# Kernel optimization log

Measured on AMD Instinct MI355X. Metric: run time of the kernel, lower is better.

Reference implementation:

```python
import jax, jax.numpy as jnp
import numpy as np

ROUTE_NUM = 3
EPS = 1e-8


def squash(s):
    # s: [bs, J, d2]; squash along last dim
    sq = jnp.sum(s * s, axis=-1, keepdims=True)
    return (sq / (1.0 + sq)) * s / jnp.sqrt(sq + EPS)


def setup_inputs() -> dict:
    key = jax.random.key(0)
    k1, k2, k3 = jax.random.split(key, 3)
    bs, in_dim, s1 = 64, 256, 16
    out_dim, J = 32, 64           # J = num_out_caps (as_final_output)
    I = s1 * s1                   # num_in_caps = 256
    x = jax.random.normal(k1, (bs, in_dim, s1, s1), dtype=jnp.float32)
    b_init = jax.random.uniform(k2, (bs, J, I), dtype=jnp.float32)
    W = jax.random.normal(k3, (out_dim * J, in_dim), dtype=jnp.float32) * 0.05
    Wb = jnp.zeros((out_dim * J,), dtype=jnp.float32)
    return {"x": x, "b_init": b_init, "W": W, "Wb": Wb}


def reference(x, b_init, W, Wb):
    bs = x.shape[0]
    J, I = b_init.shape[1], b_init.shape[2]
    d2 = W.shape[0] // J
    # 1x1 conv == per-pixel GEMM: [bs, OUT, s1, s1]
    pred = jnp.einsum('oi,bihw->bohw', W, x) + Wb[None, :, None, None]
    # [bs, J, d2, I] -> [bs, I, J, d2]
    pred = pred.reshape(bs, J, d2, I).transpose(0, 3, 1, 2)
    b = b_init
    v = None
    for _ in range(ROUTE_NUM):
        c = jax.nn.softmax(b, axis=1)                  # softmax over out-caps J
        s = jnp.einsum('bji,bijd->bjd', c, pred)       # weighted sum over in-caps
        v = squash(s)                                  # [bs, J, d2]
        db = jax.lax.stop_gradient(jnp.einsum('bjd,bijd->bji', v, pred))
        b = b + db
    return v
```

## Files before the change

### kernel.cpp

```cpp
#include <hip/hip_runtime.h>
#include <hip/hip_bf16.h>

#define BS    64
#define KDIM  256
#define ICAP  256
#define JCAP  64
#define D2    32
#define OUTD  2048
#define NPART 16

typedef short bf16x8 __attribute__((ext_vector_type(8)));
typedef float f32x4  __attribute__((ext_vector_type(4)));

static __device__ __forceinline__ float bf2f(unsigned u16) {
  union { unsigned u; float f; } v; v.u = u16 << 16; return v.f;
}
static __device__ __forceinline__ unsigned short f2bf(float x) {
  union { float f; unsigned u; } v; v.f = x;
  unsigned r = v.u + 0x7fffu + ((v.u >> 16) & 1u);
  return (unsigned short)(r >> 16);
}
static __device__ __forceinline__ void unpack8(uint4 u, float* f) {
  f[0] = bf2f(u.x & 0xffffu); f[1] = bf2f(u.x >> 16);
  f[2] = bf2f(u.y & 0xffffu); f[3] = bf2f(u.y >> 16);
  f[4] = bf2f(u.z & 0xffffu); f[5] = bf2f(u.z >> 16);
  f[6] = bf2f(u.w & 0xffffu); f[7] = bf2f(u.w >> 16);
}
static __device__ __forceinline__ void gl_lds16(const unsigned short* g,
                                                unsigned short* l) {
  __builtin_amdgcn_global_load_lds(
      (const __attribute__((address_space(1))) unsigned int*)g,
      (__attribute__((address_space(3))) unsigned int*)l, 16, 0, 0);
}

__global__ __launch_bounds__(256) void prep(
    const float* __restrict__ W, const float* __restrict__ x,
    const float* __restrict__ Binit,
    unsigned short* __restrict__ Wbf, unsigned short* __restrict__ xT,
    unsigned short* __restrict__ c0)
{
  __shared__ union {
    float Ls[64][65];
    float Bs[64][68];
  } sm;
  const int t   = threadIdx.x;
  const int blk = blockIdx.x;

  if (blk < 256) {
    const int g = blk * 256 + t;
    const float* s = W + (size_t)g * 8;
    f32x4 a = *(const f32x4*)s;
    f32x4 b = *(const f32x4*)(s + 4);
    uint4 o;
    o.x = (unsigned)f2bf(a.x) | ((unsigned)f2bf(a.y) << 16);
    o.y = (unsigned)f2bf(a.z) | ((unsigned)f2bf(a.w) << 16);
    o.z = (unsigned)f2bf(b.x) | ((unsigned)f2bf(b.y) << 16);
    o.w = (unsigned)f2bf(b.z) | ((unsigned)f2bf(b.w) << 16);
    *(uint4*)(Wbf + (size_t)g * 8) = o;
  } else if (blk < 1280) {
    const int bid = blk - 256;
    const int i0  = (bid & 3) * 64;
    const int k0  = ((bid >> 2) & 3) * 64;
    const int b   = bid >> 4;
    for (int it = 0; it < 4; ++it) {
      const int k  = it * 16 + (t >> 4);
      const int i4 = (t & 15) * 4;
      f32x4 v = *(const f32x4*)(x + ((size_t)(b * KDIM + k0 + k) * ICAP) + i0 + i4);
      sm.Ls[k][i4 + 0] = v.x; sm.Ls[k][i4 + 1] = v.y;
      sm.Ls[k][i4 + 2] = v.z; sm.Ls[k][i4 + 3] = v.w;
    }
    __syncthreads();
    const int i  = t >> 2;
    const int kc = (t & 3) * 16;
    unsigned pk[8];
    for (int q = 0; q < 8; ++q) {
      float lo = sm.Ls[kc + 2 * q][i];
      float hi = sm.Ls[kc + 2 * q + 1][i];
      pk[q] = (unsigned)f2bf(lo) | ((unsigned)f2bf(hi) << 16);
    }
    unsigned short* dst = xT + ((size_t)(b * ICAP + i0 + i) * KDIM) + k0 + kc;
    uint4 s0; s0.x = pk[0]; s0.y = pk[1]; s0.z = pk[2]; s0.w = pk[3];
    uint4 s1; s1.x = pk[4]; s1.y = pk[5]; s1.z = pk[6]; s1.w = pk[7];
    *(uint4*)dst       = s0;
    *(uint4*)(dst + 8) = s1;
  } else {
    const int bid = blk - 1280;
    const int b   = bid >> 2;
    const int q   = bid & 3;
    {
      const int j  = t >> 2;
      const int c4 = (t & 3) * 16;
      const float* src = Binit + ((size_t)(b * JCAP + j) * ICAP) + q * 64 + c4;
      for (int r = 0; r < 4; ++r) {
        f32x4 v = *(const f32x4*)(src + r * 4);
        *(f32x4*)&sm.Bs[j][c4 + r * 4] = v;
      }
    }
    __syncthreads();
    if (t < 64) {
      const int ii = t;
      float m = -3.0e38f;
      for (int j = 0; j < 64; ++j) m = fmaxf(m, sm.Bs[j][ii]);
      float se = 0.f;
      for (int j = 0; j < 64; ++j) se += __expf(sm.Bs[j][ii] - m);
      const float inv = 1.0f / se;
      unsigned short* dst = c0 + ((size_t)(b * ICAP + q * 64 + ii) * JCAP);
      for (int qq = 0; qq < 8; ++qq) {
        unsigned pk[4];
        for (int h = 0; h < 4; ++h) {
          float lo = __expf(sm.Bs[qq * 8 + 2 * h][ii] - m) * inv;
          float hi = __expf(sm.Bs[qq * 8 + 2 * h + 1][ii] - m) * inv;
          pk[h] = (unsigned)f2bf(lo) | ((unsigned)f2bf(hi) << 16);
        }
        uint4 s; s.x = pk[0]; s.y = pk[1]; s.z = pk[2]; s.w = pk[3];
        *(uint4*)(dst + qq * 8) = s;
      }
    }
  }
}

__global__ __launch_bounds__(256) void gemm_pred(
    const unsigned short* __restrict__ Wbf,
    const unsigned short* __restrict__ xT,
    const float* __restrict__ Wb,
    const unsigned short* __restrict__ c0,
    unsigned short* __restrict__ P,
    float* __restrict__ s0part)
{
  __shared__ union {
    unsigned short AB[2][128][64];
    struct {
      unsigned short C[128][136];
      unsigned short c0t[128][4];
    } ep;
  } sm;

  const int tid = threadIdx.x;
  const int b   = blockIdx.z;
  const int o0  = blockIdx.x * 128;
  const int i0  = blockIdx.y * 128;
  const int l   = tid & 63;
  const int m   = l & 15;
  const int w   = tid >> 6;
  const int wo  = (w & 1) * 64;
  const int wi  = (w >> 1) * 64;

  const int srow = l >> 3;
  const int gch  = (l & 7) ^ srow;

  f32x4 acc[4][4];
  for (int a = 0; a < 4; ++a)
    for (int c = 0; c < 4; ++c) acc[a][c] = (f32x4){0.f, 0.f, 0.f, 0.f};

  for (int r = 0; r < 4; ++r) {
    const int k0 = r * 64;
    __syncthreads();
    for (int c = 0; c < 4; ++c) {
      const int q   = w * 4 + c;
      const int row = q * 8 + srow;
      gl_lds16(Wbf + (size_t)(o0 + row) * KDIM + k0 + gch * 8,
               &sm.AB[0][q * 8][0]);
      gl_lds16(xT + ((size_t)(b * ICAP + i0 + row) * KDIM) + k0 + gch * 8,
               &sm.AB[1][q * 8][0]);
    }
    __syncthreads();
    for (int ks = 0; ks < 2; ++ks) {
      const int clog = ks * 4 + (l >> 4);
      bf16x8 af[4], bfg[4];
      for (int ti = 0; ti < 4; ++ti) {
        const int row = wo + 16 * ti + m;
        af[ti] = *(const bf16x8*)&sm.AB[0][row][(clog ^ (m & 7)) * 8];
      }
      for (int tj = 0; tj < 4; ++tj) {
        const int row = wi + 16 * tj + m;
        bfg[tj] = *(const bf16x8*)&sm.AB[1][row][(clog ^ (m & 7)) * 8];
      }
      for (int ti = 0; ti < 4; ++ti)
        for (int tj = 0; tj < 4; ++tj)
          acc[ti][tj] = __builtin_amdgcn_mfma_f32_16x16x32_bf16(
              af[ti], bfg[tj], acc[ti][tj], 0, 0, 0);
    }
  }

  __syncthreads();
  {
    const int q4 = (l >> 4) * 4;
    for (int ti = 0; ti < 4; ++ti) {
      const int ob = wo + 16 * ti + q4;
      f32x4 wb4 = *(const f32x4*)(Wb + o0 + ob);
      for (int tj = 0; tj < 4; ++tj) {
        const int ii = wi + 16 * tj + m;
        f32x4 a = acc[ti][tj];
        uint2 pk;
        pk.x = (unsigned)f2bf(a.x + wb4.x) | ((unsigned)f2bf(a.y + wb4.y) << 16);
        pk.y = (unsigned)f2bf(a.z + wb4.z) | ((unsigned)f2bf(a.w + wb4.w) << 16);
        *(uint2*)&sm.ep.C[ii][ob] = pk;
      }
    }
  }
  if (tid < 128) {
    const int j0 = blockIdx.x * 4;
    uint2 v = *(const uint2*)(c0 + ((size_t)(b * ICAP + i0 + tid) * JCAP) + j0);
    *(uint2*)&sm.ep.c0t[tid][0] = v;
  }
  __syncthreads();
  for (int rr = 0; rr < 8; ++rr) {
    const int id  = rr * 256 + tid;
    const int row = id >> 4;
    const int seg = id & 15;
    uint4 v = *(const uint4*)&sm.ep.C[row][seg * 8];
    *(uint4*)(P + ((size_t)(b * ICAP + i0 + row) * OUTD) + o0 + seg * 8) = v;
  }
  {
    const int oc = tid & 127;
    const int h  = tid >> 7;
    const int jj = oc >> 5;
    float s = 0.f;
    for (int ii = 0; ii < 64; ++ii) {
      const int i = h * 64 + ii;
      s += bf2f(sm.ep.C[i][oc]) * bf2f(sm.ep.c0t[i][jj]);
    }
    const int p = blockIdx.y * 2 + h;
    s0part[((size_t)(b * 4 + p) * OUTD) + o0 + oc] = s;
  }
}

__global__ __launch_bounds__(256) void route_fused(
    const unsigned short* __restrict__ P,
    const float* __restrict__ Binit,
    float* __restrict__ B1,
    const float* __restrict__ part_in,
    const int npart_in,
    float* __restrict__ part_out,
    const int pass)
{
  __shared__ union {
    float Vs[2112];
    float Ps[4][2112];
  } sm;

  const int tid = threadIdx.x;
  const int l   = tid & 63;
  const int w   = tid >> 6;
  const int b   = blockIdx.x >> 4;
  const int g   = blockIdx.x & 15;

  {
    const float* base = part_in + (size_t)b * npart_in * OUTD + tid * 8;
    float s[8] = {0.f,0.f,0.f,0.f,0.f,0.f,0.f,0.f};
    for (int p = 0; p < npart_in; ++p) {
      f32x4 a = *(const f32x4*)(base + (size_t)p * OUTD);
      f32x4 c = *(const f32x4*)(base + (size_t)p * OUTD + 4);
      s[0] += a.x; s[1] += a.y; s[2] += a.z; s[3] += a.w;
      s[4] += c.x; s[5] += c.y; s[6] += c.z; s[7] += c.w;
    }
    float sq = 0.f;
    for (int c = 0; c < 8; ++c) sq += s[c] * s[c];
    sq += __shfl_xor(sq, 1, 64);
    sq += __shfl_xor(sq, 2, 64);
    float scale = (sq / (1.0f + sq)) / sqrtf(sq + 1e-8f);
    const int j  = tid >> 2;
    const int d0 = (tid & 3) * 8;
    for (int c = 0; c < 8; ++c) sm.Vs[j * 33 + d0 + c] = scale * s[c];
  }
  __syncthreads();
  float vv[32];
  for (int k = 0; k < 32; ++k) vv[k] = sm.Vs[l * 33 + k];

  const int i0 = g * 16 + w * 4;
  float bold[4];
  if (pass == 1) {
    f32x4 t = *(const f32x4*)(Binit + (size_t)(b * JCAP + l) * ICAP + i0);
    bold[0] = t.x; bold[1] = t.y; bold[2] = t.z; bold[3] = t.w;
  } else {
    for (int ii = 0; ii < 4; ++ii)
      bold[ii] = B1[((size_t)(b * ICAP + i0 + ii)) * JCAP + l];
  }

  float sacc[32];
  for (int k = 0; k < 32; ++k) sacc[k] = 0.f;

  const unsigned short* pbase = P + ((size_t)(b * ICAP + i0) * OUTD) + l * D2;
  uint4 ubuf[2][4];
  for (int q = 0; q < 4; ++q) ubuf[0][q] = *(const uint4*)(pbase + q * 8);
  for (int q = 0; q < 4; ++q) ubuf[1][q] = *(const uint4*)(pbase + OUTD + q * 8);

#pragma unroll
  for (int ii = 0; ii < 4; ++ii) {
    uint4 cur[4];
    for (int q = 0; q < 4; ++q) cur[q] = ubuf[ii & 1][q];
    if (ii + 2 < 4)
      for (int q = 0; q < 4; ++q)
        ubuf[ii & 1][q] = *(const uint4*)(pbase + (size_t)(ii + 2) * OUTD + q * 8);

    float db = 0.f;
    for (int q = 0; q < 4; ++q) {
      float ps[8]; unpack8(cur[q], ps);
      for (int k = 0; k < 8; ++k) db += ps[k] * vv[q * 8 + k];
    }
    float bnew = bold[ii] + db;
    if (pass == 1) B1[((size_t)(b * ICAP + i0 + ii)) * JCAP + l] = bnew;

    float mx = bnew;
    for (int off = 1; off < 64; off <<= 1) mx = fmaxf(mx, __shfl_xor(mx, off, 64));
    float e = __expf(bnew - mx);
    float se = e;
    for (int off = 1; off < 64; off <<= 1) se += __shfl_xor(se, off, 64);
    float c = e / se;
    for (int q = 0; q < 4; ++q) {
      float ps[8]; unpack8(cur[q], ps);
      for (int k = 0; k < 8; ++k) sacc[q * 8 + k] += c * ps[k];
    }
  }

  __syncthreads();
  for (int k = 0; k < 32; ++k) sm.Ps[w][l * 33 + k] = sacc[k];
  __syncthreads();

  {
    const int o0 = tid * 8;
    float s[8];
    for (int c = 0; c < 8; ++c) {
      const int o = o0 + c, j = o >> 5, d = o & 31, idx = j * 33 + d;
      s[c] = sm.Ps[0][idx] + sm.Ps[1][idx] + sm.Ps[2][idx] + sm.Ps[3][idx];
    }
    float* dst = part_out + ((size_t)(b * NPART + g)) * OUTD + o0;
    f32x4 t0 = {s[0], s[1], s[2], s[3]};
    f32x4 t1 = {s[4], s[5], s[6], s[7]};
    *(f32x4*)dst       = t0;
    *(f32x4*)(dst + 4) = t1;
  }
}

__global__ __launch_bounds__(256) void squash_final(
    const float* __restrict__ part,
    float* __restrict__ outp)
{
  const int tid = threadIdx.x;
  const int b   = blockIdx.x;
  const float* base = part + (size_t)b * NPART * OUTD + tid * 8;
  float s[8] = {0.f,0.f,0.f,0.f,0.f,0.f,0.f,0.f};
  for (int p = 0; p < NPART; ++p) {
    f32x4 a = *(const f32x4*)(base + (size_t)p * OUTD);
    f32x4 c = *(const f32x4*)(base + (size_t)p * OUTD + 4);
    s[0] += a.x; s[1] += a.y; s[2] += a.z; s[3] += a.w;
    s[4] += c.x; s[5] += c.y; s[6] += c.z; s[7] += c.w;
  }
  float sq = 0.f;
  for (int c = 0; c < 8; ++c) sq += s[c] * s[c];
  sq += __shfl_xor(sq, 1, 64);
  sq += __shfl_xor(sq, 2, 64);
  float scale = (sq / (1.0f + sq)) / sqrtf(sq + 1e-8f);
  float* dst = outp + (size_t)b * OUTD + tid * 8;
  f32x4 t0 = {scale*s[0], scale*s[1], scale*s[2], scale*s[3]};
  f32x4 t1 = {scale*s[4], scale*s[5], scale*s[6], scale*s[7]};
  *(f32x4*)dst       = t0;
  *(f32x4*)(dst + 4) = t1;
}

extern "C" void kernel_launch(void* const* d_in, const int* in_sizes, int n_in,
                              void* d_out, int out_size, void* d_ws, size_t ws_size,
                              hipStream_t stream) {
  const float* x  = (const float*)d_in[0];
  const float* bi = (const float*)d_in[1];
  const float* W  = (const float*)d_in[2];
  const float* Wb = (const float*)d_in[3];
  float* out = (float*)d_out;

  char* ws = (char*)d_ws;
  const size_t MiB = 1024 * 1024;
  unsigned short* P        = (unsigned short*)ws;
  unsigned short* xT       = (unsigned short*)(ws + 64 * MiB);
  float*          partial1 = (float*)(ws + 64 * MiB);
  unsigned short* Wbf      = (unsigned short*)(ws + 72 * MiB);
  unsigned short* c0       = (unsigned short*)(ws + 73 * MiB);
  float*          s0part   = (float*)(ws + 75 * MiB);
  float*          partial2 = (float*)(ws + 72 * MiB);
  float* B1                = (float*)(ws + 80 * MiB);

  prep<<<dim3(1536), 256, 0, stream>>>(W, x, bi, Wbf, xT, c0);
  gemm_pred<<<dim3(16, 2, 64), 256, 0, stream>>>(Wbf, xT, Wb, c0, P, s0part);
  route_fused<<<dim3(1024), 256, 0, stream>>>(P, bi, B1, s0part, 4, partial1, 1);
  route_fused<<<dim3(1024), 256, 0, stream>>>(P, bi, B1, partial1, NPART, partial2, 2);
  squash_final<<<dim3(64), 256, 0, stream>>>(partial2, out);
}
```

Baseline: 157.5 us.

## Avoid materializing prediction tensor by reassociating routing through x and W

The old version built the full bf16 prediction tensor P [bs, I, OUT] with a GEMM and streamed it twice during routing. The new version reassociates the algebra. s = W·(x·cᵀ) + Wb·Σc is computed via a small MFMA product of x with the coupling matrix followed by a W contraction. The logit update db = (vᵀW)·x is computed by forming U = vᵀW, split into hi/lo bf16 parts, and then running an MFMA against xT. This removes the 64 MiB intermediate and its memory traffic, at the cost of more kernel launches (nine instead of five), only 256-block grids, and some scalar W-contraction loops.

New measurement: 206.8 us. 1.31x slower.

```diff
diff --git a/kernel.cpp b/kernel.cpp
--- a/kernel.cpp
+++ b/kernel.cpp
@@ -1,5 +1,4 @@
 #include <hip/hip_runtime.h>
-#include <hip/hip_bf16.h>
 
 #define BS    64
 #define KDIM  256
@@ -7,7 +6,6 @@
 #define JCAP  64
 #define D2    32
 #define OUTD  2048
-#define NPART 16
 
 typedef short bf16x8 __attribute__((ext_vector_type(8)));
 typedef float f32x4  __attribute__((ext_vector_type(4)));
@@ -26,22 +24,17 @@
   f[4] = bf2f(u.z & 0xffffu); f[5] = bf2f(u.z >> 16);
   f[6] = bf2f(u.w & 0xffffu); f[7] = bf2f(u.w >> 16);
 }
-static __device__ __forceinline__ void gl_lds16(const unsigned short* g,
-                                                unsigned short* l) {
-  __builtin_amdgcn_global_load_lds(
-      (const __attribute__((address_space(1))) unsigned int*)g,
-      (__attribute__((address_space(3))) unsigned int*)l, 16, 0, 0);
-}
 
 __global__ __launch_bounds__(256) void prep(
     const float* __restrict__ W, const float* __restrict__ x,
     const float* __restrict__ Binit,
     unsigned short* __restrict__ Wbf, unsigned short* __restrict__ xT,
-    unsigned short* __restrict__ c0)
+    unsigned short* __restrict__ xKI, unsigned short* __restrict__ c0,
+    float* __restrict__ cpart)
 {
   __shared__ union {
     float Ls[64][65];
-    float Bs[64][68];
+    struct { float Bs[64][68]; float mx[64]; float inv[64]; } S;
   } sm;
   const int t   = threadIdx.x;
   const int blk = blockIdx.x;
@@ -70,19 +63,36 @@
       sm.Ls[k][i4 + 2] = v.z; sm.Ls[k][i4 + 3] = v.w;
     }
     __syncthreads();
-    const int i  = t >> 2;
-    const int kc = (t & 3) * 16;
-    unsigned pk[8];
-    for (int q = 0; q < 8; ++q) {
-      float lo = sm.Ls[kc + 2 * q][i];
-      float hi = sm.Ls[kc + 2 * q + 1][i];
-      pk[q] = (unsigned)f2bf(lo) | ((unsigned)f2bf(hi) << 16);
-    }
-    unsigned short* dst = xT + ((size_t)(b * ICAP + i0 + i) * KDIM) + k0 + kc;
-    uint4 s0; s0.x = pk[0]; s0.y = pk[1]; s0.z = pk[2]; s0.w = pk[3];
-    uint4 s1; s1.x = pk[4]; s1.y = pk[5]; s1.z = pk[6]; s1.w = pk[7];
-    *(uint4*)dst       = s0;
-    *(uint4*)(dst + 8) = s1;
+    {
+      const int i  = t >> 2;
+      const int kc = (t & 3) * 16;
+      unsigned pk[8];
+      for (int q = 0; q < 8; ++q) {
+        float lo = sm.Ls[kc + 2 * q][i];
+        float hi = sm.Ls[kc + 2 * q + 1][i];
+        pk[q] = (unsigned)f2bf(lo) | ((unsigned)f2bf(hi) << 16);
+      }
+      unsigned short* dst = xT + ((size_t)(b * ICAP + i0 + i) * KDIM) + k0 + kc;
+      uint4 s0; s0.x = pk[0]; s0.y = pk[1]; s0.z = pk[2]; s0.w = pk[3];
+      uint4 s1; s1.x = pk[4]; s1.y = pk[5]; s1.z = pk[6]; s1.w = pk[7];
+      *(uint4*)dst       = s0;
+      *(uint4*)(dst + 8) = s1;
+    }
+    {
+      const int k   = t >> 2;
+      const int ic4 = (t & 3) * 16;
+      unsigned pk[8];
+      for (int h = 0; h < 8; ++h) {
+        float lo = sm.Ls[k][ic4 + 2 * h];
+        float hi = sm.Ls[k][ic4 + 2 * h + 1];
+        pk[h] = (unsigned)f2bf(lo) | ((unsigned)f2bf(hi) << 16);
+      }
+      unsigned short* dst = xKI + ((size_t)(b * KDIM + k0 + k) * ICAP) + i0 + ic4;
+      uint4 s0; s0.x = pk[0]; s0.y = pk[1]; s0.z = pk[2]; s0.w = pk[3];
+      uint4 s1; s1.x = pk[4]; s1.y = pk[5]; s1.z = pk[6]; s1.w = pk[7];
+      *(uint4*)dst       = s0;
+      *(uint4*)(dst + 8) = s1;
+    }
   } else {
     const int bid = blk - 1280;
     const int b   = bid >> 2;
@@ -91,269 +101,331 @@
       const int j  = t >> 2;
       const int c4 = (t & 3) * 16;
       const float* src = Binit + ((size_t)(b * JCAP + j) * ICAP) + q * 64 + c4;
-      for (int r = 0; r < 4; ++r) {
-        f32x4 v = *(const f32x4*)(src + r * 4);
-        *(f32x4*)&sm.Bs[j][c4 + r * 4] = v;
-      }
+      for (int r = 0; r < 4; ++r)
+        *(f32x4*)&sm.S.Bs[j][c4 + r * 4] = *(const f32x4*)(src + r * 4);
     }
     __syncthreads();
     if (t < 64) {
       const int ii = t;
       float m = -3.0e38f;
-      for (int j = 0; j < 64; ++j) m = fmaxf(m, sm.Bs[j][ii]);
+      for (int j = 0; j < 64; ++j) m = fmaxf(m, sm.S.Bs[j][ii]);
       float se = 0.f;
-      for (int j = 0; j < 64; ++j) se += __expf(sm.Bs[j][ii] - m);
-      const float inv = 1.0f / se;
-      unsigned short* dst = c0 + ((size_t)(b * ICAP + q * 64 + ii) * JCAP);
-      for (int qq = 0; qq < 8; ++qq) {
-        unsigned pk[4];
-        for (int h = 0; h < 4; ++h) {
-          float lo = __expf(sm.Bs[qq * 8 + 2 * h][ii] - m) * inv;
-          float hi = __expf(sm.Bs[qq * 8 + 2 * h + 1][ii] - m) * inv;
-          pk[h] = (unsigned)f2bf(lo) | ((unsigned)f2bf(hi) << 16);
-        }
-        uint4 s; s.x = pk[0]; s.y = pk[1]; s.z = pk[2]; s.w = pk[3];
-        *(uint4*)(dst + qq * 8) = s;
+      for (int j = 0; j < 64; ++j) se += __expf(sm.S.Bs[j][ii] - m);
+      sm.S.mx[ii]  = m;
+      sm.S.inv[ii] = 1.0f / se;
+    }
+    __syncthreads();
+    {
+      const int j  = t >> 2;
+      const int c4 = (t & 3) * 16;
+      float cs = 0.f;
+      unsigned pk[8];
+      for (int h = 0; h < 8; ++h) {
+        const int i0 = c4 + 2 * h;
+        float lo = __expf(sm.S.Bs[j][i0]     - sm.S.mx[i0])     * sm.S.inv[i0];
+        float hi = __expf(sm.S.Bs[j][i0 + 1] - sm.S.mx[i0 + 1]) * sm.S.inv[i0 + 1];
+        cs += lo + hi;
+        pk[h] = (unsigned)f2bf(lo) | ((unsigned)f2bf(hi) << 16);
       }
-    }
-  }
-}
-
-__global__ __launch_bounds__(256) void gemm_pred(
+      unsigned short* dst = c0 + ((size_t)(b * JCAP + j) * ICAP) + q * 64 + c4;
+      uint4 s0; s0.x = pk[0]; s0.y = pk[1]; s0.z = pk[2]; s0.w = pk[3];
+      uint4 s1; s1.x = pk[4]; s1.y = pk[5]; s1.z = pk[6]; s1.w = pk[7];
+      *(uint4*)dst       = s0;
+      *(uint4*)(dst + 8) = s1;
+      cs += __shfl_xor(cs, 1, 64);
+      cs += __shfl_xor(cs, 2, 64);
+      if ((t & 3) == 0) cpart[((size_t)(b * 4 + q)) * JCAP + j] = cs;
+    }
+  }
+}
+
+__global__ __launch_bounds__(256) void k_sv(
+    const unsigned short* __restrict__ xKI,
+    const unsigned short* __restrict__ cmat,
     const unsigned short* __restrict__ Wbf,
-    const unsigned short* __restrict__ xT,
-    const float* __restrict__ Wb,
-    const unsigned short* __restrict__ c0,
-    unsigned short* __restrict__ P,
-    float* __restrict__ s0part)
+    float* __restrict__ spart)
 {
-  __shared__ union {
-    unsigned short AB[2][128][64];
-    struct {
-      unsigned short C[128][136];
-      unsigned short c0t[128][4];
-    } ep;
-  } sm;
-
+  __shared__ float Y[64][68];
   const int tid = threadIdx.x;
-  const int b   = blockIdx.z;
-  const int o0  = blockIdx.x * 128;
-  const int i0  = blockIdx.y * 128;
-  const int l   = tid & 63;
-  const int m   = l & 15;
-  const int w   = tid >> 6;
-  const int wo  = (w & 1) * 64;
-  const int wi  = (w >> 1) * 64;
-
-  const int srow = l >> 3;
-  const int gch  = (l & 7) ^ srow;
-
-  f32x4 acc[4][4];
-  for (int a = 0; a < 4; ++a)
-    for (int c = 0; c < 4; ++c) acc[a][c] = (f32x4){0.f, 0.f, 0.f, 0.f};
-
-  for (int r = 0; r < 4; ++r) {
-    const int k0 = r * 64;
-    __syncthreads();
-    for (int c = 0; c < 4; ++c) {
-      const int q   = w * 4 + c;
-      const int row = q * 8 + srow;
-      gl_lds16(Wbf + (size_t)(o0 + row) * KDIM + k0 + gch * 8,
-               &sm.AB[0][q * 8][0]);
-      gl_lds16(xT + ((size_t)(b * ICAP + i0 + row) * KDIM) + k0 + gch * 8,
-               &sm.AB[1][q * 8][0]);
-    }
-    __syncthreads();
-    for (int ks = 0; ks < 2; ++ks) {
-      const int clog = ks * 4 + (l >> 4);
-      bf16x8 af[4], bfg[4];
-      for (int ti = 0; ti < 4; ++ti) {
-        const int row = wo + 16 * ti + m;
-        af[ti] = *(const bf16x8*)&sm.AB[0][row][(clog ^ (m & 7)) * 8];
-      }
-      for (int tj = 0; tj < 4; ++tj) {
-        const int row = wi + 16 * tj + m;
-        bfg[tj] = *(const bf16x8*)&sm.AB[1][row][(clog ^ (m & 7)) * 8];
-      }
-      for (int ti = 0; ti < 4; ++ti)
-        for (int tj = 0; tj < 4; ++tj)
-          acc[ti][tj] = __builtin_amdgcn_mfma_f32_16x16x32_bf16(
-              af[ti], bfg[tj], acc[ti][tj], 0, 0, 0);
-    }
-  }
-
-  __syncthreads();
-  {
-    const int q4 = (l >> 4) * 4;
-    for (int ti = 0; ti < 4; ++ti) {
-      const int ob = wo + 16 * ti + q4;
-      f32x4 wb4 = *(const f32x4*)(Wb + o0 + ob);
-      for (int tj = 0; tj < 4; ++tj) {
-        const int ii = wi + 16 * tj + m;
-        f32x4 a = acc[ti][tj];
-        uint2 pk;
-        pk.x = (unsigned)f2bf(a.x + wb4.x) | ((unsigned)f2bf(a.y + wb4.y) << 16);
-        pk.y = (unsigned)f2bf(a.z + wb4.z) | ((unsigned)f2bf(a.w + wb4.w) << 16);
-        *(uint2*)&sm.ep.C[ii][ob] = pk;
-      }
-    }
-  }
-  if (tid < 128) {
-    const int j0 = blockIdx.x * 4;
-    uint2 v = *(const uint2*)(c0 + ((size_t)(b * ICAP + i0 + tid) * JCAP) + j0);
-    *(uint2*)&sm.ep.c0t[tid][0] = v;
-  }
-  __syncthreads();
-  for (int rr = 0; rr < 8; ++rr) {
-    const int id  = rr * 256 + tid;
-    const int row = id >> 4;
-    const int seg = id & 15;
-    uint4 v = *(const uint4*)&sm.ep.C[row][seg * 8];
-    *(uint4*)(P + ((size_t)(b * ICAP + i0 + row) * OUTD) + o0 + seg * 8) = v;
-  }
-  {
-    const int oc = tid & 127;
-    const int h  = tid >> 7;
-    const int jj = oc >> 5;
-    float s = 0.f;
-    for (int ii = 0; ii < 64; ++ii) {
-      const int i = h * 64 + ii;
-      s += bf2f(sm.ep.C[i][oc]) * bf2f(sm.ep.c0t[i][jj]);
-    }
-    const int p = blockIdx.y * 2 + h;
-    s0part[((size_t)(b * 4 + p) * OUTD) + o0 + oc] = s;
-  }
-}
-
-__global__ __launch_bounds__(256) void route_fused(
-    const unsigned short* __restrict__ P,
-    const float* __restrict__ Binit,
-    float* __restrict__ B1,
-    const float* __restrict__ part_in,
-    const int npart_in,
-    float* __restrict__ part_out,
-    const int pass)
-{
-  __shared__ union {
-    float Vs[2112];
-    float Ps[4][2112];
-  } sm;
-
-  const int tid = threadIdx.x;
+  const int b   = blockIdx.x >> 2;
+  const int kc  = blockIdx.x & 3;
   const int l   = tid & 63;
   const int w   = tid >> 6;
-  const int b   = blockIdx.x >> 4;
-  const int g   = blockIdx.x & 15;
-
+
+  f32x4 acc[4];
+  for (int n = 0; n < 4; ++n) acc[n] = (f32x4){0.f, 0.f, 0.f, 0.f};
+
+  const unsigned short* Ap =
+      xKI + ((size_t)(b * KDIM + kc * 64 + w * 16 + (l & 15))) * ICAP + (l >> 4) * 8;
+  const unsigned short* Bp =
+      cmat + ((size_t)(b * JCAP + (l & 15))) * ICAP + (l >> 4) * 8;
+#pragma unroll
+  for (int ks = 0; ks < 8; ++ks) {
+    bf16x8 a = *(const bf16x8*)(Ap + ks * 32);
+#pragma unroll
+    for (int n = 0; n < 4; ++n) {
+      bf16x8 bb = *(const bf16x8*)(Bp + (size_t)n * 16 * ICAP + ks * 32);
+      acc[n] = __builtin_amdgcn_mfma_f32_16x16x32_bf16(a, bb, acc[n], 0, 0, 0);
+    }
+  }
+#pragma unroll
+  for (int n = 0; n < 4; ++n)
+#pragma unroll
+    for (int r = 0; r < 4; ++r)
+      Y[w * 16 + (l >> 4) * 4 + r][n * 16 + (l & 15)] = acc[n][r];
+  __syncthreads();
+
+  const int j = tid >> 2;
+  float sacc[8];
+#pragma unroll
+  for (int d = 0; d < 8; ++d) sacc[d] = 0.f;
+  const unsigned short* wbase = Wbf + (size_t)(tid * 8) * KDIM + kc * 64;
+  for (int k8 = 0; k8 < 8; ++k8) {
+    float y8[8];
+#pragma unroll
+    for (int e = 0; e < 8; ++e) y8[e] = Y[k8 * 8 + e][j];
+#pragma unroll
+    for (int d = 0; d < 8; ++d) {
+      uint4 u = *(const uint4*)(wbase + (size_t)d * KDIM + k8 * 8);
+      float f[8]; unpack8(u, f);
+      float s = sacc[d];
+#pragma unroll
+      for (int e = 0; e < 8; ++e) s += f[e] * y8[e];
+      sacc[d] = s;
+    }
+  }
+  float* dst = spart + ((size_t)(b * 4 + kc)) * OUTD + tid * 8;
+  f32x4 t0 = {sacc[0], sacc[1], sacc[2], sacc[3]};
+  f32x4 t1 = {sacc[4], sacc[5], sacc[6], sacc[7]};
+  *(f32x4*)dst       = t0;
+  *(f32x4*)(dst + 4) = t1;
+}
+
+__global__ __launch_bounds__(256) void k_u(
+    const float* __restrict__ spart, const float* __restrict__ cpart,
+    const float* __restrict__ Wb, const unsigned short* __restrict__ Wbf,
+    unsigned short* __restrict__ Uhi, unsigned short* __restrict__ Ulo)
+{
+  __shared__ float vls[JCAP * 33];
+  const int tid = threadIdx.x;
+  const int b   = blockIdx.x >> 2;
+  const int kc  = blockIdx.x & 3;
+  const int j   = tid >> 2;
   {
-    const float* base = part_in + (size_t)b * npart_in * OUTD + tid * 8;
-    float s[8] = {0.f,0.f,0.f,0.f,0.f,0.f,0.f,0.f};
-    for (int p = 0; p < npart_in; ++p) {
-      f32x4 a = *(const f32x4*)(base + (size_t)p * OUTD);
-      f32x4 c = *(const f32x4*)(base + (size_t)p * OUTD + 4);
-      s[0] += a.x; s[1] += a.y; s[2] += a.z; s[3] += a.w;
-      s[4] += c.x; s[5] += c.y; s[6] += c.z; s[7] += c.w;
-    }
+    const float* sp = spart + (size_t)b * 4 * OUTD + tid * 8;
+    f32x4 a0 = *(const f32x4*)sp;
+    f32x4 a1 = *(const f32x4*)(sp + 4);
+    for (int p = 1; p < 4; ++p) {
+      a0 += *(const f32x4*)(sp + (size_t)p * OUTD);
+      a1 += *(const f32x4*)(sp + (size_t)p * OUTD + 4);
+    }
+    float cs = cpart[((size_t)b * 4) * JCAP + j] + cpart[((size_t)(b * 4 + 1)) * JCAP + j] +
+               cpart[((size_t)(b * 4 + 2)) * JCAP + j] + cpart[((size_t)(b * 4 + 3)) * JCAP + j];
+    f32x4 wb0 = *(const f32x4*)(Wb + tid * 8);
+    f32x4 wb1 = *(const f32x4*)(Wb + tid * 8 + 4);
+    float s8[8];
+    s8[0] = a0.x + cs * wb0.x; s8[1] = a0.y + cs * wb0.y;
+    s8[2] = a0.z + cs * wb0.z; s8[3] = a0.w + cs * wb0.w;
+    s8[4] = a1.x + cs * wb1.x; s8[5] = a1.y + cs * wb1.y;
+    s8[6] = a1.z + cs * wb1.z; s8[7] = a1.w + cs * wb1.w;
     float sq = 0.f;
-    for (int c = 0; c < 8; ++c) sq += s[c] * s[c];
+    for (int e = 0; e < 8; ++e) sq += s8[e] * s8[e];
     sq += __shfl_xor(sq, 1, 64);
     sq += __shfl_xor(sq, 2, 64);
     float scale = (sq / (1.0f + sq)) / sqrtf(sq + 1e-8f);
-    const int j  = tid >> 2;
     const int d0 = (tid & 3) * 8;
-    for (int c = 0; c < 8; ++c) sm.Vs[j * 33 + d0 + c] = scale * s[c];
+    for (int e = 0; e < 8; ++e) vls[j * 33 + d0 + e] = scale * s8[e];
   }
   __syncthreads();
-  float vv[32];
-  for (int k = 0; k < 32; ++k) vv[k] = sm.Vs[l * 33 + k];
-
-  const int i0 = g * 16 + w * 4;
-  float bold[4];
+
+  const int kg = kc * 64 + (tid & 3) * 16;
+  float acc[16];
+#pragma unroll
+  for (int e = 0; e < 16; ++e) acc[e] = 0.f;
+  const float* vj = vls + j * 33;
+  const unsigned short* wrow = Wbf + (size_t)(j * D2) * KDIM + kg;
+  for (int d = 0; d < 32; ++d) {
+    float vd = vj[d];
+    uint4 u0 = *(const uint4*)(wrow + (size_t)d * KDIM);
+    uint4 u1 = *(const uint4*)(wrow + (size_t)d * KDIM + 8);
+    float f[16]; unpack8(u0, f); unpack8(u1, f + 8);
+#pragma unroll
+    for (int e = 0; e < 16; ++e) acc[e] += vd * f[e];
+  }
+  unsigned ph[8], pl[8];
+  for (int h = 0; h < 8; ++h) {
+    unsigned short h0 = f2bf(acc[2 * h]), h1 = f2bf(acc[2 * h + 1]);
+    float r0 = acc[2 * h] - bf2f(h0), r1 = acc[2 * h + 1] - bf2f(h1);
+    ph[h] = (unsigned)h0 | ((unsigned)h1 << 16);
+    pl[h] = (unsigned)f2bf(r0) | ((unsigned)f2bf(r1) << 16);
+  }
+  size_t off = ((size_t)(b * JCAP + j)) * KDIM + kg;
+  uint4 q0; q0.x = ph[0]; q0.y = ph[1]; q0.z = ph[2]; q0.w = ph[3];
+  uint4 q1; q1.x = ph[4]; q1.y = ph[5]; q1.z = ph[6]; q1.w = ph[7];
+  *(uint4*)(Uhi + off)     = q0;
+  *(uint4*)(Uhi + off + 8) = q1;
+  uint4 q2; q2.x = pl[0]; q2.y = pl[1]; q2.z = pl[2]; q2.w = pl[3];
+  uint4 q3; q3.x = pl[4]; q3.y = pl[5]; q3.z = pl[6]; q3.w = pl[7];
+  *(uint4*)(Ulo + off)     = q2;
+  *(uint4*)(Ulo + off + 8) = q3;
+}
+
+__global__ __launch_bounds__(256) void k_db(
+    const unsigned short* __restrict__ xT,
+    const unsigned short* __restrict__ Uhi, const unsigned short* __restrict__ Ulo,
+    const float* __restrict__ spart, const float* __restrict__ cpart_in,
+    const float* __restrict__ Wb,
+    const float* __restrict__ Binit,
+    float* __restrict__ blog,
+    unsigned short* __restrict__ cmat,
+    float* __restrict__ cpart_out,
+    const int pass)
+{
+  __shared__ struct {
+    float dbl[64][68];
+    float ub[64];
+    unsigned short ct[64][66];
+    float cpw[4][66];
+  } sm;
+  const int tid = threadIdx.x;
+  const int b   = blockIdx.x >> 2;
+  const int ic  = blockIdx.x & 3;
+  const int i0  = ic * 64;
+  const int l   = tid & 63;
+  const int w   = tid >> 6;
+
+  {
+    const float* sp = spart + (size_t)b * 4 * OUTD + tid * 8;
+    f32x4 a0 = *(const f32x4*)sp;
+    f32x4 a1 = *(const f32x4*)(sp + 4);
+    for (int p = 1; p < 4; ++p) {
+      a0 += *(const f32x4*)(sp + (size_t)p * OUTD);
+      a1 += *(const f32x4*)(sp + (size_t)p * OUTD + 4);
+    }
+    const int j = tid >> 2;
+    float cs = cpart_in[((size_t)b * 4) * JCAP + j] + cpart_in[((size_t)(b * 4 + 1)) * JCAP + j] +
+               cpart_in[((size_t)(b * 4 + 2)) * JCAP + j] + cpart_in[((size_t)(b * 4 + 3)) * JCAP + j];
+    f32x4 wb0 = *(const f32x4*)(Wb + tid * 8);
+    f32x4 wb1 = *(const f32x4*)(Wb + tid * 8 + 4);
+    float s8[8];
+    s8[0] = a0.x + cs * wb0.x; s8[1] = a0.y + cs * wb0.y;
+    s8[2] = a0.z + cs * wb0.z; s8[3] = a0.w + cs * wb0.w;
+    s8[4] = a1.x + cs * wb1.x; s8[5] = a1.y + cs * wb1.y;
+    s8[6] = a1.z + cs * wb1.z; s8[7] = a1.w + cs * wb1.w;
+    float sq = 0.f;
+    for (int e = 0; e < 8; ++e) sq += s8[e] * s8[e];
+    sq += __shfl_xor(sq, 1, 64);
+    sq += __shfl_xor(sq, 2, 64);
+    float scale = (sq / (1.0f + sq)) / sqrtf(sq + 1e-8f);
+    float ub = scale * (s8[0] * wb0.x + s8[1] * wb0.y + s8[2] * wb0.z + s8[3] * wb0.w +
+                        s8[4] * wb1.x + s8[5] * wb1.y + s8[6] * wb1.z + s8[7] * wb1.w);
+    ub += __shfl_xor(ub, 1, 64);
+    ub += __shfl_xor(ub, 2, 64);
+    if ((tid & 3) == 0) sm.ub[j] = ub;
+  }
+
+  f32x4 acc[4];
+  for (int n = 0; n < 4; ++n) acc[n] = (f32x4){0.f, 0.f, 0.f, 0.f};
+  const unsigned short* Ap =
+      xT + ((size_t)(b * ICAP + i0 + w * 16 + (l & 15))) * KDIM + (l >> 4) * 8;
+  const unsigned short* Bh = Uhi + ((size_t)(b * JCAP + (l & 15))) * KDIM + (l >> 4) * 8;
+  const unsigned short* Bl = Ulo + ((size_t)(b * JCAP + (l & 15))) * KDIM + (l >> 4) * 8;
+#pragma unroll
+  for (int ks = 0; ks < 8; ++ks) {
+    bf16x8 a = *(const bf16x8*)(Ap + ks * 32);
+#pragma unroll
+    for (int n = 0; n < 4; ++n) {
+      bf16x8 bh = *(const bf16x8*)(Bh + (size_t)n * 16 * KDIM + ks * 32);
+      acc[n] = __builtin_amdgcn_mfma_f32_16x16x32_bf16(a, bh, acc[n], 0, 0, 0);
+      bf16x8 bl = *(const bf16x8*)(Bl + (size_t)n * 16 * KDIM + ks * 32);
+      acc[n] = __builtin_amdgcn_mfma_f32_16x16x32_bf16(a, bl, acc[n], 0, 0, 0);
+    }
+  }
+#pragma unroll
+  for (int n = 0; n < 4; ++n)
+#pragma unroll
+    for (int r = 0; r < 4; ++r)
+      sm.dbl[w * 16 + (l >> 4) * 4 + r][n * 16 + (l & 15)] = acc[n][r];
+  __syncthreads();
+
+  float bold[16];
   if (pass == 1) {
-    f32x4 t = *(const f32x4*)(Binit + (size_t)(b * JCAP + l) * ICAP + i0);
-    bold[0] = t.x; bold[1] = t.y; bold[2] = t.z; bold[3] = t.w;
+    const float* src = Binit + ((size_t)(b * JCAP + l)) * ICAP + i0 + w * 16;
+    for (int r = 0; r < 4; ++r) {
+      f32x4 v = *(const f32x4*)(src + r * 4);
+      bold[r * 4 + 0] = v.x; bold[r * 4 + 1] = v.y;
+      bold[r * 4 + 2] = v.z; bold[r * 4 + 3] = v.w;
+    }
   } else {
-    for (int ii = 0; ii < 4; ++ii)
-      bold[ii] = B1[((size_t)(b * ICAP + i0 + ii)) * JCAP + l];
-  }
-
-  float sacc[32];
-  for (int k = 0; k < 32; ++k) sacc[k] = 0.f;
-
-  const unsigned short* pbase = P + ((size_t)(b * ICAP + i0) * OUTD) + l * D2;
-  uint4 ubuf[2][4];
-  for (int q = 0; q < 4; ++q) ubuf[0][q] = *(const uint4*)(pbase + q * 8);
-  for (int q = 0; q < 4; ++q) ubuf[1][q] = *(const uint4*)(pbase + OUTD + q * 8);
-
-#pragma unroll
-  for (int ii = 0; ii < 4; ++ii) {
-    uint4 cur[4];
-    for (int q = 0; q < 4; ++q) cur[q] = ubuf[ii & 1][q];
-    if (ii + 2 < 4)
-      for (int q = 0; q < 4; ++q)
-        ubuf[ii & 1][q] = *(const uint4*)(pbase + (size_t)(ii + 2) * OUTD + q * 8);
-
-    float db = 0.f;
-    for (int q = 0; q < 4; ++q) {
-      float ps[8]; unpack8(cur[q], ps);
-      for (int k = 0; k < 8; ++k) db += ps[k] * vv[q * 8 + k];
-    }
-    float bnew = bold[ii] + db;
-    if (pass == 1) B1[((size_t)(b * ICAP + i0 + ii)) * JCAP + l] = bnew;
-
-    float mx = bnew;
+    for (int ii = 0; ii < 16; ++ii)
+      bold[ii] = blog[((size_t)(b * ICAP + i0 + w * 16 + ii)) * JCAP + l];
+  }
+  float csl = 0.f;
+  const float ubl = sm.ub[l];
+  for (int ii = 0; ii < 16; ++ii) {
+    float bn = bold[ii] + sm.dbl[w * 16 + ii][l] + ubl;
+    if (pass == 1)
+      blog[((size_t)(b * ICAP + i0 + w * 16 + ii)) * JCAP + l] = bn;
+    float mx = bn;
     for (int off = 1; off < 64; off <<= 1) mx = fmaxf(mx, __shfl_xor(mx, off, 64));
-    float e = __expf(bnew - mx);
+    float e = __expf(bn - mx);
     float se = e;
     for (int off = 1; off < 64; off <<= 1) se += __shfl_xor(se, off, 64);
     float c = e / se;
-    for (int q = 0; q < 4; ++q) {
-      float ps[8]; unpack8(cur[q], ps);
-      for (int k = 0; k < 8; ++k) sacc[q * 8 + k] += c * ps[k];
-    }
-  }
-
+    sm.ct[l][w * 16 + ii] = f2bf(c);
+    csl += c;
+  }
+  sm.cpw[w][l] = csl;
   __syncthreads();
-  for (int k = 0; k < 32; ++k) sm.Ps[w][l * 33 + k] = sacc[k];
-  __syncthreads();
 
   {
-    const int o0 = tid * 8;
-    float s[8];
-    for (int c = 0; c < 8; ++c) {
-      const int o = o0 + c, j = o >> 5, d = o & 31, idx = j * 33 + d;
-      s[c] = sm.Ps[0][idx] + sm.Ps[1][idx] + sm.Ps[2][idx] + sm.Ps[3][idx];
-    }
-    float* dst = part_out + ((size_t)(b * NPART + g)) * OUTD + o0;
-    f32x4 t0 = {s[0], s[1], s[2], s[3]};
-    f32x4 t1 = {s[4], s[5], s[6], s[7]};
-    *(f32x4*)dst       = t0;
-    *(f32x4*)(dst + 4) = t1;
-  }
-}
-
-__global__ __launch_bounds__(256) void squash_final(
-    const float* __restrict__ part,
-    float* __restrict__ outp)
+    const int j  = tid >> 2;
+    const int ch = (tid & 3) * 16;
+    unsigned pk[8];
+    for (int h = 0; h < 8; ++h)
+      pk[h] = *(const unsigned*)&sm.ct[j][ch + 2 * h];
+    unsigned short* dst = cmat + ((size_t)(b * JCAP + j)) * ICAP + i0 + ch;
+    uint4 s0; s0.x = pk[0]; s0.y = pk[1]; s0.z = pk[2]; s0.w = pk[3];
+    uint4 s1; s1.x = pk[4]; s1.y = pk[5]; s1.z = pk[6]; s1.w = pk[7];
+    *(uint4*)dst       = s0;
+    *(uint4*)(dst + 8) = s1;
+  }
+  if (tid < 64)
+    cpart_out[((size_t)(b * 4 + ic)) * JCAP + tid] =
+        sm.cpw[0][tid] + sm.cpw[1][tid] + sm.cpw[2][tid] + sm.cpw[3][tid];
+}
+
+__global__ __launch_bounds__(256) void k_final(
+    const float* __restrict__ spart, const float* __restrict__ cpart,
+    const float* __restrict__ Wb, float* __restrict__ outp)
 {
   const int tid = threadIdx.x;
   const int b   = blockIdx.x;
-  const float* base = part + (size_t)b * NPART * OUTD + tid * 8;
-  float s[8] = {0.f,0.f,0.f,0.f,0.f,0.f,0.f,0.f};
-  for (int p = 0; p < NPART; ++p) {
-    f32x4 a = *(const f32x4*)(base + (size_t)p * OUTD);
-    f32x4 c = *(const f32x4*)(base + (size_t)p * OUTD + 4);
-    s[0] += a.x; s[1] += a.y; s[2] += a.z; s[3] += a.w;
-    s[4] += c.x; s[5] += c.y; s[6] += c.z; s[7] += c.w;
-  }
+  const float* sp = spart + (size_t)b * 4 * OUTD + tid * 8;
+  f32x4 a0 = *(const f32x4*)sp;
+  f32x4 a1 = *(const f32x4*)(sp + 4);
+  for (int p = 1; p < 4; ++p) {
+    a0 += *(const f32x4*)(sp + (size_t)p * OUTD);
+    a1 += *(const f32x4*)(sp + (size_t)p * OUTD + 4);
+  }
+  const int j = tid >> 2;
+  float cs = cpart[((size_t)b * 4) * JCAP + j] + cpart[((size_t)(b * 4 + 1)) * JCAP + j] +
+             cpart[((size_t)(b * 4 + 2)) * JCAP + j] + cpart[((size_t)(b * 4 + 3)) * JCAP + j];
+  f32x4 wb0 = *(const f32x4*)(Wb + tid * 8);
+  f32x4 wb1 = *(const f32x4*)(Wb + tid * 8 + 4);
+  float s8[8];
+  s8[0] = a0.x + cs * wb0.x; s8[1] = a0.y + cs * wb0.y;
+  s8[2] = a0.z + cs * wb0.z; s8[3] = a0.w + cs * wb0.w;
+  s8[4] = a1.x + cs * wb1.x; s8[5] = a1.y + cs * wb1.y;
+  s8[6] = a1.z + cs * wb1.z; s8[7] = a1.w + cs * wb1.w;
   float sq = 0.f;
-  for (int c = 0; c < 8; ++c) sq += s[c] * s[c];
+  for (int e = 0; e < 8; ++e) sq += s8[e] * s8[e];
   sq += __shfl_xor(sq, 1, 64);
   sq += __shfl_xor(sq, 2, 64);
   float scale = (sq / (1.0f + sq)) / sqrtf(sq + 1e-8f);
   float* dst = outp + (size_t)b * OUTD + tid * 8;
-  f32x4 t0 = {scale*s[0], scale*s[1], scale*s[2], scale*s[3]};
-  f32x4 t1 = {scale*s[4], scale*s[5], scale*s[6], scale*s[7]};
+  f32x4 t0 = {scale * s8[0], scale * s8[1], scale * s8[2], scale * s8[3]};
+  f32x4 t1 = {scale * s8[4], scale * s8[5], scale * s8[6], scale * s8[7]};
   *(f32x4*)dst       = t0;
   *(f32x4*)(dst + 4) = t1;
 }
@@ -369,18 +441,24 @@
 
   char* ws = (char*)d_ws;
   const size_t MiB = 1024 * 1024;
-  unsigned short* P        = (unsigned short*)ws;
-  unsigned short* xT       = (unsigned short*)(ws + 64 * MiB);
-  float*          partial1 = (float*)(ws + 64 * MiB);
-  unsigned short* Wbf      = (unsigned short*)(ws + 72 * MiB);
-  unsigned short* c0       = (unsigned short*)(ws + 73 * MiB);
-  float*          s0part   = (float*)(ws + 75 * MiB);
-  float*          partial2 = (float*)(ws + 72 * MiB);
-  float* B1                = (float*)(ws + 80 * MiB);
-
-  prep<<<dim3(1536), 256, 0, stream>>>(W, x, bi, Wbf, xT, c0);
-  gemm_pred<<<dim3(16, 2, 64), 256, 0, stream>>>(Wbf, xT, Wb, c0, P, s0part);
-  route_fused<<<dim3(1024), 256, 0, stream>>>(P, bi, B1, s0part, 4, partial1, 1);
-  route_fused<<<dim3(1024), 256, 0, stream>>>(P, bi, B1, partial1, NPART, partial2, 2);
-  squash_final<<<dim3(64), 256, 0, stream>>>(partial2, out);
-}
+  unsigned short* xT     = (unsigned short*)(ws + 0 * MiB);
+  unsigned short* xKI    = (unsigned short*)(ws + 8 * MiB);
+  unsigned short* Wbf    = (unsigned short*)(ws + 16 * MiB);
+  unsigned short* cm     = (unsigned short*)(ws + 17 * MiB);
+  unsigned short* Uhi    = (unsigned short*)(ws + 19 * MiB);
+  unsigned short* Ulo    = (unsigned short*)(ws + 21 * MiB);
+  float*          spart  = (float*)(ws + 23 * MiB);
+  float*          blog   = (float*)(ws + 25 * MiB);
+  float*          cpartA = (float*)(ws + 29 * MiB);
+  float*          cpartB = (float*)(ws + 30 * MiB);
+
+  prep<<<dim3(1536), 256, 0, stream>>>(W, x, bi, Wbf, xT, xKI, cm, cpartA);
+  k_sv<<<dim3(256), 256, 0, stream>>>(xKI, cm, Wbf, spart);
+  k_u <<<dim3(256), 256, 0, stream>>>(spart, cpartA, Wb, Wbf, Uhi, Ulo);
+  k_db<<<dim3(256), 256, 0, stream>>>(xT, Uhi, Ulo, spart, cpartA, Wb, bi, blog, cm, cpartB, 1);
+  k_sv<<<dim3(256), 256, 0, stream>>>(xKI, cm, Wbf, spart);
+  k_u <<<dim3(256), 256, 0, stream>>>(spart, cpartB, Wb, Wbf, Uhi, Ulo);
+  k_db<<<dim3(256), 256, 0, stream>>>(xT, Uhi, Ulo, spart, cpartB, Wb, bi, blog, cm, cpartA, 2);
+  k_sv<<<dim3(256), 256, 0, stream>>>(xKI, cm, Wbf, spart);
+  k_final<<<dim3(64), 256, 0, stream>>>(spart, cpartA, Wb, out);
+}
```
